# Kernel tuning notes

Hardware: AMD Instinct MI355X
Metric: run time of the kernel (lower is better)

Reference implementation:

```python
import jax, jax.numpy as jnp
import numpy as np

B, C, CO = 8, 32, 32            # batch, in_channels, out_channels
NIN, NOUT, D1, D2 = 16, 10, 512, 512  # MLP dims: 16 -> 512 -> 512 -> 10 (L=3)
NRC = (NIN + 2 * NOUT + 6) * C  # rc_inp feature dim = 42*C = 1344


def _conv1(x, W, b):
    # 1x1 Conv1d: x (b, Cin, N) -> (b, Cout, N)
    return jnp.einsum('oi,bin->bon', W, x) + b[None, :, None]


def _lin(x, W, b):
    return x @ W.T + b


def setup_inputs() -> dict:
    key = jax.random.key(0)
    ks = iter(jax.random.split(key, 64))
    def rn(shape, s=1.0):
        return jax.random.normal(next(ks), shape, dtype=jnp.float32) * s
    return {
        'w0': rn((B, C, D1, NIN)), 'w1': rn((B, C, D2, D1)), 'w2': rn((B, C, NOUT, D2)),
        'b0': rn((B, C, D1)), 'b1': rn((B, C, D2)), 'b2': rn((B, C, NOUT)),
        'W_w0_rpt': rn((NIN * CO, (NIN + 2) * C), 0.02), 'B_w0_rpt': rn((NIN * CO,), 0.02),
        'W_w0_rc': rn((NIN * CO, NRC), 0.02), 'B_w0_rc': rn((NIN * CO,), 0.02),
        'W_b0': rn((CO, (NIN + 2) * C), 0.02), 'B_b0': rn((CO,), 0.02),
        'W_b0_rc': rn((CO, NRC), 0.02), 'B_b0_rc': rn((CO,), 0.02),
        'W_l1': rn((CO, C), 0.02), 'B_l1': rn((CO,), 0.02),
        'W_l1_rc': rn((CO, NRC), 0.02), 'B_l1_rc': rn((CO,), 0.02),
        'W_l1_r': rn((CO, (3 + NIN) * C), 0.02), 'B_l1_r': rn((CO,), 0.02),
        'W_l1_c': rn((CO, (3 + NOUT) * C), 0.02), 'B_l1_c': rn((CO,), 0.02),
        'W_bias1': rn((CO, (3 + NOUT) * C), 0.02), 'B_bias1': rn((CO,), 0.02),
        'W_bias1_rc': rn((CO, NRC), 0.02), 'B_bias1_rc': rn((CO,), 0.02),
        'W_fin_cpt': rn((NOUT * CO, (NOUT + 1) * C), 0.02), 'B_fin_cpt': rn((NOUT * CO,), 0.02),
        'W_fin_rc': rn((NOUT * CO, NRC), 0.02), 'B_fin_rc': rn((NOUT * CO,), 0.02),
        'W_bfin_rc': rn((NOUT * CO, NRC), 0.02), 'B_bfin_rc': rn((NOUT * CO,), 0.02),
    }


def reference(w0, w1, w2, b0, b1, b2,
              W_w0_rpt, B_w0_rpt, W_w0_rc, B_w0_rc, W_b0, B_b0, W_b0_rc, B_b0_rc,
              W_l1, B_l1, W_l1_rc, B_l1_rc, W_l1_r, B_l1_r, W_l1_c, B_l1_c,
              W_bias1, B_bias1, W_bias1_rc, B_bias1_rc,
              W_fin_cpt, B_fin_cpt, W_fin_rc, B_fin_rc, W_bfin_rc, B_bfin_rc):
    b = w0.shape[0]
    cm0, cm1, cm2 = w0.mean(-1), w1.mean(-1), w2.mean(-1)  # col means (b,c,n_row)
    rm0, rm1, rm2 = w0.mean(-2), w1.mean(-2), w2.mean(-2)  # row means (b,c,n_col)
    rc = jnp.concatenate([
        w0.mean((-1, -2)), w1.mean((-1, -2)), w2.mean((-1, -2)),
        b0.mean(-1), b1.mean(-1), b2.mean(-1),
        rm0.reshape(b, -1), cm2.reshape(b, -1), b2.reshape(b, -1)], axis=-1)  # (b, NRC)
    # ---- layer 0 (row-pointwise + rc broadcast) ----
    rpt = jnp.concatenate([jnp.swapaxes(w0, -1, -2).reshape(b, C * NIN, D1), rm1, b0], axis=1)
    z0 = _conv1(rpt, W_w0_rpt, B_w0_rpt) + _lin(rc, W_w0_rc, B_w0_rc)[..., None]
    zw0 = jnp.swapaxes(z0.reshape(b, CO, NIN, D1), -1, -2)  # (b, co, D1, NIN)
    u0 = _conv1(rpt, W_b0, B_b0) + _lin(rc, W_b0_rc, B_b0_rc)[..., None]  # (b, co, D1)
    # ---- middle layer (pointwise + rc + row + col broadcasts) ----
    row_b = jnp.concatenate([rm1, cm0, b0, jnp.swapaxes(w0, -1, -2).reshape(b, C * NIN, D1)], axis=1)
    col_b = jnp.concatenate([cm1, b1, rm2, w2.reshape(b, C * NOUT, D2)], axis=1)
    zw1 = (jnp.einsum('oi,bihw->bohw', W_l1, w1) + B_l1[None, :, None, None]
           + _lin(rc, W_l1_rc, B_l1_rc)[..., None, None]
           + _conv1(row_b, W_l1_r, B_l1_r)[:, :, None, :]
           + _conv1(col_b, W_l1_c, B_l1_c)[:, :, :, None])  # (b, co, D2, D1)
    u1 = _conv1(col_b, W_bias1, B_bias1) + _lin(rc, W_bias1_rc, B_bias1_rc)[..., None]  # (b, co, D2)
    # ---- final layer (col-pointwise + rc broadcast) ----
    cpt = jnp.concatenate([w2.reshape(b, C * NOUT, D2), cm1], axis=1)
    zf = _conv1(cpt, W_fin_cpt, B_fin_cpt) + _lin(rc, W_fin_rc, B_fin_rc)[..., None]
    zw2 = zf.reshape(b, CO, NOUT, D2)
    u2 = _lin(rc, W_bfin_rc, B_bfin_rc).reshape(b, CO, NOUT)
    return (zw0, zw1, zw2, u0, u1, u2)
```

## Files before the change

### kernel.cpp

```cpp
#include <hip/hip_runtime.h>

#define OUT_ZW1 2097152u
#define OUT_ZW2 69206016u
#define OUT_U0  70516736u
#define OUT_U1  70647808u
#define OUT_U2  70778880u

#define WS_RM1P   0u
#define WS_CM1    524288u
#define WS_CM0    655360u
#define WS_RM2    786432u
#define WS_RCW1   917504u
#define WS_RC     918528u
#define WS_RTERM  929280u
#define WS_CTERM  1060352u
#define WS_W0T    1191424u
#define WS_TW0    3288576u
#define WS_TB0    3292672u
#define WS_TL1    3292928u
#define WS_TBIAS1 3293184u
#define WS_TFIN   3293440u

static __device__ __forceinline__ float wave_reduce(float v) {
#pragma unroll
  for (int off = 32; off > 0; off >>= 1) v += __shfl_down(v, off);
  return v;
}

__global__ __launch_bounds__(256) void ksetup(
    const float* __restrict__ w0, const float* __restrict__ w2,
    const float* __restrict__ b0, const float* __restrict__ b1,
    const float* __restrict__ b2, const float* __restrict__ w1,
    float* __restrict__ ws) {
  __shared__ float sred[16];
  __shared__ float stot;
  __shared__ float rpart[512];
  __shared__ float swsum[4];
  int tid = threadIdx.x, lane = tid & 63;
  int bx = blockIdx.x;

  if (bx < 256) {
    int bc = bx;
    int b = bc >> 5, c = bc & 31;
    float* rcb = ws + WS_RC + b * 1344;
    float* cm0 = ws + WS_CM0;
    float* rm2 = ws + WS_RM2;

    if (tid < 16) sred[tid] = 0.f;
    if (tid == 0) stot = 0.f;
    __syncthreads();
    {
      float rm0p[16];
#pragma unroll
      for (int k = 0; k < 16; ++k) rm0p[k] = 0.f;
      float tot = 0.f;
      for (int d = tid; d < 512; d += 256) {
        const float4* p = (const float4*)(w0 + ((size_t)bc * 512 + d) * 16);
        float s = 0.f;
#pragma unroll
        for (int q = 0; q < 4; ++q) {
          float4 v = p[q];
          s += v.x + v.y + v.z + v.w;
          rm0p[q * 4 + 0] += v.x; rm0p[q * 4 + 1] += v.y;
          rm0p[q * 4 + 2] += v.z; rm0p[q * 4 + 3] += v.w;
        }
        cm0[(size_t)bc * 512 + d] = s * (1.f / 16.f);
        tot += s;
      }
#pragma unroll
      for (int k = 0; k < 16; ++k) {
        float r = wave_reduce(rm0p[k]);
        if (lane == 0) atomicAdd(&sred[k], r);
      }
      float rt = wave_reduce(tot);
      if (lane == 0) atomicAdd(&stot, rt);
    }
    __syncthreads();
    if (tid < 16) rcb[192 + c * 16 + tid] = sred[tid] * (1.f / 512.f);
    if (tid == 0) rcb[c] = stot * (1.f / 8192.f);
    __syncthreads();

    if (tid < 10) sred[tid] = 0.f;
    if (tid == 0) stot = 0.f;
    __syncthreads();
    {
      float cm2p[10];
#pragma unroll
      for (int k = 0; k < 10; ++k) cm2p[k] = 0.f;
      float tot = 0.f;
      for (int d = tid; d < 512; d += 256) {
        float s = 0.f;
#pragma unroll
        for (int k = 0; k < 10; ++k) {
          float v = w2[((size_t)bc * 10 + k) * 512 + d];
          s += v; cm2p[k] += v;
        }
        rm2[(size_t)bc * 512 + d] = s * 0.1f;
        tot += s;
      }
#pragma unroll
      for (int k = 0; k < 10; ++k) {
        float r = wave_reduce(cm2p[k]);
        if (lane == 0) atomicAdd(&sred[k], r);
      }
      float rt = wave_reduce(tot);
      if (lane == 0) atomicAdd(&stot, rt);
    }
    __syncthreads();
    if (tid < 10) rcb[704 + c * 10 + tid] = sred[tid] * (1.f / 512.f);
    if (tid == 0) rcb[64 + c] = stot * (1.f / 5120.f);
    __syncthreads();

    if (tid < 2) sred[tid] = 0.f;
    __syncthreads();
    {
      float t0 = 0.f, t1 = 0.f;
      for (int d = tid; d < 512; d += 256) {
        t0 += b0[(size_t)bc * 512 + d];
        t1 += b1[(size_t)bc * 512 + d];
      }
      t0 = wave_reduce(t0); t1 = wave_reduce(t1);
      if (lane == 0) { atomicAdd(&sred[0], t0); atomicAdd(&sred[1], t1); }
    }
    __syncthreads();
    if (tid == 0) {
      rcb[96 + c] = sred[0] * (1.f / 512.f);
      rcb[128 + c] = sred[1] * (1.f / 512.f);
    }

    float vb2 = 0.f;
    if (tid < 10) {
      vb2 = b2[bc * 10 + tid];
      rcb[1024 + c * 10 + tid] = vb2;
    }
    if (tid < 64) {
      float s = wave_reduce(vb2);
      if (tid == 0) rcb[160 + c] = s * 0.1f;
    }
  } else if (bx < 1280) {
    int idx = bx - 256;
    int bc = idx >> 2, hc = idx & 3;
    int wid = tid >> 6;
    const float* base = w1 + (size_t)bc * 262144 + (size_t)hc * 65536;
    float col0 = 0.f, col1 = 0.f;
    for (int hl = 0; hl < 128; ++hl) {
      float2 x = *(const float2*)(base + hl * 512 + 2 * tid);
      col0 += x.x; col1 += x.y;
      float r = wave_reduce(x.x + x.y);
      if (lane == 0) rpart[hl * 4 + wid] = r;
    }
    __syncthreads();
    if (tid < 128) {
      float s = rpart[tid * 4] + rpart[tid * 4 + 1] + rpart[tid * 4 + 2] + rpart[tid * 4 + 3];
      ws[WS_CM1 + (size_t)bc * 512 + hc * 128 + tid] = s * (1.f / 512.f);
    }
    ws[WS_RM1P + (size_t)hc * 131072 + (size_t)bc * 512 + 2 * tid] = col0;
    ws[WS_RM1P + (size_t)hc * 131072 + (size_t)bc * 512 + 2 * tid + 1] = col1;
    float bt = wave_reduce(col0 + col1);
    if (lane == 0) swsum[wid] = bt;
    __syncthreads();
    if (tid == 0)
      ws[WS_RCW1 + hc * 256 + bc] = swsum[0] + swsum[1] + swsum[2] + swsum[3];
  } else {
    int bc = bx - 1280;
    int b = bc >> 5, c = bc & 31;
    for (int dd = 0; dd < 2; ++dd) {
      int d = tid + dd * 256;
      const float4* src = (const float4*)(w0 + ((size_t)bc * 512 + d) * 16);
      float4 v0 = src[0], v1 = src[1], v2 = src[2], v3 = src[3];
      float vals[16] = {v0.x, v0.y, v0.z, v0.w, v1.x, v1.y, v1.z, v1.w,
                        v2.x, v2.y, v2.z, v2.w, v3.x, v3.y, v3.z, v3.w};
#pragma unroll
      for (int k = 0; k < 16; ++k)
        ws[WS_W0T + ((size_t)(b * 512 + c * 16 + k)) * 512 + d] = vals[k];
    }
  }
}

__global__ __launch_bounds__(256) void krcgemm(
    float* __restrict__ ws,
    const float* __restrict__ W_w0_rc, const float* __restrict__ B_w0_rc,
    const float* __restrict__ W_b0_rc, const float* __restrict__ B_b0_rc,
    const float* __restrict__ W_l1_rc, const float* __restrict__ B_l1_rc,
    const float* __restrict__ W_bias1_rc, const float* __restrict__ B_bias1_rc,
    const float* __restrict__ W_fin_rc, const float* __restrict__ B_fin_rc,
    const float* __restrict__ W_bfin_rc, const float* __restrict__ B_bfin_rc,
    float* __restrict__ u2out) {
  int blk = blockIdx.x, tid = threadIdx.x;
  if (blk >= 2496) {
    int i = (blk - 2496) * 256 + tid;
    ws[WS_RM1P + i] = ws[WS_RM1P + i] + ws[WS_RM1P + 131072 + i] +
                      ws[WS_RM1P + 262144 + i] + ws[WS_RM1P + 393216 + i];
    return;
  }
  int b = blk / 312;
  int lane = tid & 63, wid = tid >> 6;
  int r = (blk % 312) * 4 + wid;
  __shared__ float rcs[1344];
  for (int j = tid; j < 1344; j += 256)
    if (j < 32 || j >= 64) rcs[j] = ws[WS_RC + b * 1344 + j];
  if (tid < 32)
    rcs[32 + tid] = (ws[WS_RCW1 + 0 * 256 + b * 32 + tid] +
                     ws[WS_RCW1 + 1 * 256 + b * 32 + tid] +
                     ws[WS_RCW1 + 2 * 256 + b * 32 + tid] +
                     ws[WS_RCW1 + 3 * 256 + b * 32 + tid]) * (1.f / 262144.f);
  __syncthreads();
  const float* W; const float* Bb; float* dst; int row;
  if (r < 512)      { W = W_w0_rc;    Bb = B_w0_rc;    row = r;       dst = ws + WS_TW0 + b * 512; }
  else if (r < 544) { W = W_b0_rc;    Bb = B_b0_rc;    row = r - 512; dst = ws + WS_TB0 + b * 32; }
  else if (r < 576) { W = W_l1_rc;    Bb = B_l1_rc;    row = r - 544; dst = ws + WS_TL1 + b * 32; }
  else if (r < 608) { W = W_bias1_rc; Bb = B_bias1_rc; row = r - 576; dst = ws + WS_TBIAS1 + b * 32; }
  else if (r < 928) { W = W_fin_rc;   Bb = B_fin_rc;   row = r - 608; dst = ws + WS_TFIN + b * 320; }
  else              { W = W_bfin_rc;  Bb = B_bfin_rc;  row = r - 928; dst = u2out + b * 320; }
  const float* wr = W + (size_t)row * 1344;
  float acc = 0.f;
  for (int j = lane; j < 1344; j += 64) acc += wr[j] * rcs[j];
  acc = wave_reduce(acc);
  if (lane == 0) dst[row] = acc + Bb[row];
}

__global__ __launch_bounds__(256) void kbig(
    const float* __restrict__ rm1, const float* __restrict__ cm0,
    const float* __restrict__ b0, const float* __restrict__ w0T,
    const float* __restrict__ W_l1_r, const float* __restrict__ B_l1_r,
    float* __restrict__ rterm,
    const float* __restrict__ cm1, const float* __restrict__ b1,
    const float* __restrict__ rm2, const float* __restrict__ w2,
    const float* __restrict__ W_l1_c, const float* __restrict__ B_l1_c,
    const float* __restrict__ B_l1, const float* __restrict__ t_l1,
    const float* __restrict__ W_bias1, const float* __restrict__ B_bias1,
    const float* __restrict__ t_bias1,
    float* __restrict__ cterm_full, float* __restrict__ u1out,
    const float* __restrict__ W_w0_rpt, const float* __restrict__ B_rpt,
    const float* __restrict__ W_b0, const float* __restrict__ B_b0w,
    const float* __restrict__ t_w0, const float* __restrict__ t_b0,
    const float* __restrict__ W_fin_cpt, const float* __restrict__ B_fin,
    const float* __restrict__ t_fin, float* __restrict__ out) {
  __shared__ float wlds[6656];
  int bid = blockIdx.x, tid = threadIdx.x;

  if (bid < 128) {
    int x = bid & 1, oy = (bid >> 1) & 7, b = bid >> 4;
    int p = x * 256 + tid;
    if (oy < 4) {
      int o0 = oy * 8;
      for (int idx = tid; idx < 608 * 8; idx += 256) {
        int i = idx >> 3, oo = idx & 7;
        wlds[idx] = W_l1_r[(size_t)(o0 + oo) * 608 + i];
      }
      __syncthreads();
      float acc[8] = {0, 0, 0, 0, 0, 0, 0, 0};
#pragma unroll 4
      for (int i = 0; i < 32; ++i) {
        float xv = rm1[((size_t)b * 32 + i) * 512 + p] * (1.f / 512.f);
        float4 wa = *(const float4*)&wlds[i * 8];
        float4 wb = *(const float4*)&wlds[i * 8 + 4];
        acc[0] += wa.x * xv; acc[1] += wa.y * xv; acc[2] += wa.z * xv; acc[3] += wa.w * xv;
        acc[4] += wb.x * xv; acc[5] += wb.y * xv; acc[6] += wb.z * xv; acc[7] += wb.w * xv;
      }
#pragma unroll 4
      for (int i = 0; i < 32; ++i) {
        float xv = cm0[((size_t)b * 32 + i) * 512 + p];
        float4 wa = *(const float4*)&wlds[(32 + i) * 8];
        float4 wb = *(const float4*)&wlds[(32 + i) * 8 + 4];
        acc[0] += wa.x * xv; acc[1] += wa.y * xv; acc[2] += wa.z * xv; acc[3] += wa.w * xv;
        acc[4] += wb.x * xv; acc[5] += wb.y * xv; acc[6] += wb.z * xv; acc[7] += wb.w * xv;
      }
#pragma unroll 4
      for (int i = 0; i < 32; ++i) {
        float xv = b0[((size_t)b * 32 + i) * 512 + p];
        float4 wa = *(const float4*)&wlds[(64 + i) * 8];
        float4 wb = *(const float4*)&wlds[(64 + i) * 8 + 4];
        acc[0] += wa.x * xv; acc[1] += wa.y * xv; acc[2] += wa.z * xv; acc[3] += wa.w * xv;
        acc[4] += wb.x * xv; acc[5] += wb.y * xv; acc[6] += wb.z * xv; acc[7] += wb.w * xv;
      }
      const float* xp = w0T + (size_t)b * 512 * 512 + p;
#pragma unroll 4
      for (int i = 0; i < 512; ++i) {
        float xv = xp[(size_t)i * 512];
        float4 wa = *(const float4*)&wlds[(96 + i) * 8];
        float4 wb = *(const float4*)&wlds[(96 + i) * 8 + 4];
        acc[0] += wa.x * xv; acc[1] += wa.y * xv; acc[2] += wa.z * xv; acc[3] += wa.w * xv;
        acc[4] += wb.x * xv; acc[5] += wb.y * xv; acc[6] += wb.z * xv; acc[7] += wb.w * xv;
      }
#pragma unroll
      for (int oo = 0; oo < 8; ++oo) {
        int o = o0 + oo;
        rterm[((size_t)b * 32 + o) * 512 + p] = acc[oo] + B_l1_r[o];
      }
    } else {
      int o0 = (oy - 4) * 8;
      for (int idx = tid; idx < 416 * 8; idx += 256) {
        int i = idx >> 3, oo = idx & 7;
        wlds[idx] = W_l1_c[(size_t)(o0 + oo) * 416 + i];
        wlds[3328 + idx] = W_bias1[(size_t)(o0 + oo) * 416 + i];
      }
      __syncthreads();
      float ac[8] = {0, 0, 0, 0, 0, 0, 0, 0};
      float au[8] = {0, 0, 0, 0, 0, 0, 0, 0};
#pragma unroll 4
      for (int i = 0; i < 32; ++i) {
        float xv = cm1[((size_t)b * 32 + i) * 512 + p];
        float4 wa = *(const float4*)&wlds[i * 8];
        float4 wb = *(const float4*)&wlds[i * 8 + 4];
        float4 va = *(const float4*)&wlds[3328 + i * 8];
        float4 vb = *(const float4*)&wlds[3328 + i * 8 + 4];
        ac[0] += wa.x * xv; ac[1] += wa.y * xv; ac[2] += wa.z * xv; ac[3] += wa.w * xv;
        ac[4] += wb.x * xv; ac[5] += wb.y * xv; ac[6] += wb.z * xv; ac[7] += wb.w * xv;
        au[0] += va.x * xv; au[1] += va.y * xv; au[2] += va.z * xv; au[3] += va.w * xv;
        au[4] += vb.x * xv; au[5] += vb.y * xv; au[6] += vb.z * xv; au[7] += vb.w * xv;
      }
#pragma unroll 4
      for (int i = 0; i < 32; ++i) {
        float xv = b1[((size_t)b * 32 + i) * 512 + p];
        float4 wa = *(const float4*)&wlds[(32 + i) * 8];
        float4 wb = *(const float4*)&wlds[(32 + i) * 8 + 4];
        float4 va = *(const float4*)&wlds[3328 + (32 + i) * 8];
        float4 vb = *(const float4*)&wlds[3328 + (32 + i) * 8 + 4];
        ac[0] += wa.x * xv; ac[1] += wa.y * xv; ac[2] += wa.z * xv; ac[3] += wa.w * xv;
        ac[4] += wb.x * xv; ac[5] += wb.y * xv; ac[6] += wb.z * xv; ac[7] += wb.w * xv;
        au[0] += va.x * xv; au[1] += va.y * xv; au[2] += va.z * xv; au[3] += va.w * xv;
        au[4] += vb.x * xv; au[5] += vb.y * xv; au[6] += vb.z * xv; au[7] += vb.w * xv;
      }
#pragma unroll 4
      for (int i = 0; i < 32; ++i) {
        float xv = rm2[((size_t)b * 32 + i) * 512 + p];
        float4 wa = *(const float4*)&wlds[(64 + i) * 8];
        float4 wb = *(const float4*)&wlds[(64 + i) * 8 + 4];
        float4 va = *(const float4*)&wlds[3328 + (64 + i) * 8];
        float4 vb = *(const float4*)&wlds[3328 + (64 + i) * 8 + 4];
        ac[0] += wa.x * xv; ac[1] += wa.y * xv; ac[2] += wa.z * xv; ac[3] += wa.w * xv;
        ac[4] += wb.x * xv; ac[5] += wb.y * xv; ac[6] += wb.z * xv; ac[7] += wb.w * xv;
        au[0] += va.x * xv; au[1] += va.y * xv; au[2] += va.z * xv; au[3] += va.w * xv;
        au[4] += vb.x * xv; au[5] += vb.y * xv; au[6] += vb.z * xv; au[7] += vb.w * xv;
      }
      const float* xp = w2 + (size_t)b * 320 * 512 + p;
#pragma unroll 4
      for (int i = 0; i < 320; ++i) {
        float xv = xp[(size_t)i * 512];
        float4 wa = *(const float4*)&wlds[(96 + i) * 8];
        float4 wb = *(const float4*)&wlds[(96 + i) * 8 + 4];
        float4 va = *(const float4*)&wlds[3328 + (96 + i) * 8];
        float4 vb = *(const float4*)&wlds[3328 + (96 + i) * 8 + 4];
        ac[0] += wa.x * xv; ac[1] += wa.y * xv; ac[2] += wa.z * xv; ac[3] += wa.w * xv;
        ac[4] += wb.x * xv; ac[5] += wb.y * xv; ac[6] += wb.z * xv; ac[7] += wb.w * xv;
        au[0] += va.x * xv; au[1] += va.y * xv; au[2] += va.z * xv; au[3] += va.w * xv;
        au[4] += vb.x * xv; au[5] += vb.y * xv; au[6] += vb.z * xv; au[7] += vb.w * xv;
      }
#pragma unroll
      for (int oo = 0; oo < 8; ++oo) {
        int o = o0 + oo;
        cterm_full[((size_t)b * 32 + o) * 512 + p] = ac[oo] + B_l1_c[o] + B_l1[o] + t_l1[b * 32 + o];
        u1out[((size_t)b * 32 + o) * 512 + p] = au[oo] + B_bias1[o] + t_bias1[b * 32 + o];
      }
    }
  } else if (bid < 1216) {
    int t = bid - 128;
    int x = t & 1, rest = t >> 1;
    int oc = rest % 68, b = rest / 68;
    bool isZ = oc < 64;
    int o0 = isZ ? oc * 8 : (oc - 64) * 8;
    const float* Wsrc = isZ ? W_w0_rpt : W_b0;
    for (int idx = tid; idx < 576 * 8; idx += 256) {
      int i = idx >> 3, oo = idx & 7;
      wlds[idx] = Wsrc[(size_t)(o0 + oo) * 576 + i];
    }
    __syncthreads();
    int d = x * 256 + tid;
    float acc[8] = {0, 0, 0, 0, 0, 0, 0, 0};
    const float* xp = w0T + (size_t)b * 512 * 512 + d;
#pragma unroll 4
    for (int i = 0; i < 512; ++i) {
      float xv = xp[(size_t)i * 512];
      float4 wa = *(const float4*)&wlds[i * 8];
      float4 wb = *(const float4*)&wlds[i * 8 + 4];
      acc[0] += wa.x * xv; acc[1] += wa.y * xv; acc[2] += wa.z * xv; acc[3] += wa.w * xv;
      acc[4] += wb.x * xv; acc[5] += wb.y * xv; acc[6] += wb.z * xv; acc[7] += wb.w * xv;
    }
#pragma unroll 4
    for (int i = 0; i < 32; ++i) {
      float xv = rm1[((size_t)b * 32 + i) * 512 + d] * (1.f / 512.f);
      float4 wa = *(const float4*)&wlds[(512 + i) * 8];
      float4 wb = *(const float4*)&wlds[(512 + i) * 8 + 4];
      acc[0] += wa.x * xv; acc[1] += wa.y * xv; acc[2] += wa.z * xv; acc[3] += wa.w * xv;
      acc[4] += wb.x * xv; acc[5] += wb.y * xv; acc[6] += wb.z * xv; acc[7] += wb.w * xv;
    }
#pragma unroll 4
    for (int i = 0; i < 32; ++i) {
      float xv = b0[((size_t)b * 32 + i) * 512 + d];
      float4 wa = *(const float4*)&wlds[(544 + i) * 8];
      float4 wb = *(const float4*)&wlds[(544 + i) * 8 + 4];
      acc[0] += wa.x * xv; acc[1] += wa.y * xv; acc[2] += wa.z * xv; acc[3] += wa.w * xv;
      acc[4] += wb.x * xv; acc[5] += wb.y * xv; acc[6] += wb.z * xv; acc[7] += wb.w * xv;
    }
    if (isZ) {
#pragma unroll
      for (int oo = 0; oo < 8; ++oo) {
        int o = o0 + oo, co = o >> 4, k = o & 15;
        out[(((size_t)b * 32 + co) * 512 + d) * 16 + k] = acc[oo] + B_rpt[o] + t_w0[b * 512 + o];
      }
    } else {
#pragma unroll
      for (int oo = 0; oo < 8; ++oo) {
        int o = o0 + oo;
        out[OUT_U0 + ((size_t)b * 32 + o) * 512 + d] = acc[oo] + B_b0w[o] + t_b0[b * 32 + o];
      }
    }
  } else {
    int t = bid - 1216;
    int x = t & 1, rest = t >> 1;
    int oc = rest % 40, b = rest / 40;
    int o0 = oc * 8;
    for (int idx = tid; idx < 352 * 8; idx += 256) {
      int i = idx >> 3, oo = idx & 7;
      wlds[idx] = W_fin_cpt[(size_t)(o0 + oo) * 352 + i];
    }
    __syncthreads();
    int d = x * 256 + tid;
    float acc[8] = {0, 0, 0, 0, 0, 0, 0, 0};
    const float* xp = w2 + (size_t)b * 320 * 512 + d;
#pragma unroll 4
    for (int i = 0; i < 320; ++i) {
      float xv = xp[(size_t)i * 512];
      float4 wa = *(const float4*)&wlds[i * 8];
      float4 wb = *(const float4*)&wlds[i * 8 + 4];
      acc[0] += wa.x * xv; acc[1] += wa.y * xv; acc[2] += wa.z * xv; acc[3] += wa.w * xv;
      acc[4] += wb.x * xv; acc[5] += wb.y * xv; acc[6] += wb.z * xv; acc[7] += wb.w * xv;
    }
#pragma unroll 4
    for (int i = 0; i < 32; ++i) {
      float xv = cm1[((size_t)b * 32 + i) * 512 + d];
      float4 wa = *(const float4*)&wlds[(320 + i) * 8];
      float4 wb = *(const float4*)&wlds[(320 + i) * 8 + 4];
      acc[0] += wa.x * xv; acc[1] += wa.y * xv; acc[2] += wa.z * xv; acc[3] += wa.w * xv;
      acc[4] += wb.x * xv; acc[5] += wb.y * xv; acc[6] += wb.z * xv; acc[7] += wb.w * xv;
    }
#pragma unroll
    for (int oo = 0; oo < 8; ++oo) {
      int o = o0 + oo;
      out[OUT_ZW2 + ((size_t)b * 320 + o) * 512 + d] = acc[oo] + B_fin[o] + t_fin[b * 320 + o];
    }
  }
}

__global__ __launch_bounds__(256) void kzw1(
    const float* __restrict__ w1, const float* __restrict__ W_l1,
    const float* __restrict__ rterm, const float* __restrict__ cterm,
    float* __restrict__ out) {
  __shared__ float wl[1024];
  int hp = blockIdx.x, b = blockIdx.y;
  int t = threadIdx.x;
  for (int i = t; i < 1024; i += 256) wl[(i & 31) * 32 + (i >> 5)] = W_l1[i];
  __syncthreads();
  int h0 = hp * 2;
  int hoff = t >> 7;
  int w = (t & 127) * 4;
  float4 acc[32];
#pragma unroll
  for (int o = 0; o < 32; ++o) acc[o] = make_float4(0.f, 0.f, 0.f, 0.f);
  const float* src = w1 + ((size_t)b * 32 * 512 + h0) * 512 + 4 * t;
#pragma unroll 4
  for (int i = 0; i < 32; ++i) {
    float4 x = *(const float4*)(src + (size_t)i * 262144);
    const float* wp = wl + i * 32;
#pragma unroll
    for (int o = 0; o < 32; ++o) {
      acc[o].x += wp[o] * x.x;
      acc[o].y += wp[o] * x.y;
      acc[o].z += wp[o] * x.z;
      acc[o].w += wp[o] * x.w;
    }
  }
  int h = h0 + hoff;
#pragma unroll
  for (int o = 0; o < 32; ++o) {
    float cf = cterm[((size_t)b * 32 + o) * 512 + h];
    float4 rt = *(const float4*)(rterm + ((size_t)b * 32 + o) * 512 + w);
    float4 res = make_float4(acc[o].x + rt.x + cf, acc[o].y + rt.y + cf,
                             acc[o].z + rt.z + cf, acc[o].w + rt.w + cf);
    *(float4*)(out + (size_t)OUT_ZW1 + (((size_t)b * 32 + o) * 512 + h) * 512 + w) = res;
  }
}

extern "C" void kernel_launch(void* const* d_in, const int* in_sizes, int n_in,
                              void* d_out, int out_size, void* d_ws, size_t ws_size,
                              hipStream_t stream) {
  const float* w0 = (const float*)d_in[0];
  const float* w1 = (const float*)d_in[1];
  const float* w2 = (const float*)d_in[2];
  const float* b0 = (const float*)d_in[3];
  const float* b1 = (const float*)d_in[4];
  const float* b2 = (const float*)d_in[5];
  const float* W_w0_rpt = (const float*)d_in[6];
  const float* B_w0_rpt = (const float*)d_in[7];
  const float* W_w0_rc = (const float*)d_in[8];
  const float* B_w0_rc = (const float*)d_in[9];
  const float* W_b0 = (const float*)d_in[10];
  const float* B_b0 = (const float*)d_in[11];
  const float* W_b0_rc = (const float*)d_in[12];
  const float* B_b0_rc = (const float*)d_in[13];
  const float* W_l1 = (const float*)d_in[14];
  const float* B_l1 = (const float*)d_in[15];
  const float* W_l1_rc = (const float*)d_in[16];
  const float* B_l1_rc = (const float*)d_in[17];
  const float* W_l1_r = (const float*)d_in[18];
  const float* B_l1_r = (const float*)d_in[19];
  const float* W_l1_c = (const float*)d_in[20];
  const float* B_l1_c = (const float*)d_in[21];
  const float* W_bias1 = (const float*)d_in[22];
  const float* B_bias1 = (const float*)d_in[23];
  const float* W_bias1_rc = (const float*)d_in[24];
  const float* B_bias1_rc = (const float*)d_in[25];
  const float* W_fin_cpt = (const float*)d_in[26];
  const float* B_fin_cpt = (const float*)d_in[27];
  const float* W_fin_rc = (const float*)d_in[28];
  const float* B_fin_rc = (const float*)d_in[29];
  const float* W_bfin_rc = (const float*)d_in[30];
  const float* B_bfin_rc = (const float*)d_in[31];
  float* ws = (float*)d_ws;
  float* out = (float*)d_out;

  ksetup<<<dim3(1536), 256, 0, stream>>>(w0, w2, b0, b1, b2, w1, ws);

  krcgemm<<<dim3(3008), 256, 0, stream>>>(
      ws, W_w0_rc, B_w0_rc, W_b0_rc, B_b0_rc, W_l1_rc, B_l1_rc, W_bias1_rc,
      B_bias1_rc, W_fin_rc, B_fin_rc, W_bfin_rc, B_bfin_rc, out + OUT_U2);

  kbig<<<dim3(1856), 256, 0, stream>>>(
      ws + WS_RM1P, ws + WS_CM0, b0, ws + WS_W0T, W_l1_r, B_l1_r, ws + WS_RTERM,
      ws + WS_CM1, b1, ws + WS_RM2, w2, W_l1_c, B_l1_c, B_l1, ws + WS_TL1, W_bias1,
      B_bias1, ws + WS_TBIAS1, ws + WS_CTERM, out + OUT_U1,
      W_w0_rpt, B_w0_rpt, W_b0, B_b0, ws + WS_TW0, ws + WS_TB0,
      W_fin_cpt, B_fin_cpt, ws + WS_TFIN, out);

  kzw1<<<dim3(256, 8), 256, 0, stream>>>(w1, W_l1, ws + WS_RTERM, ws + WS_CTERM, out);
  (void)in_sizes; (void)n_in; (void)out_size; (void)ws_size;
}
```

Measured before the change: 360.7 us.

## Replace scalar FP32 conv GEMMs with bf16 MFMA GEMM over packed panels

Setup now packs the activations and weights into bf16 panels, staged in the not-yet-written zw1 region of the output buffer. The four FP32 per-thread GEMM branches are replaced by one tiled kernel that computes 64x64 tiles with 16x16x32 bf16 MFMA instructions. The aim is to move the conv-style GEMMs from scalar FMAs onto matrix cores and to halve the operand bytes read. In exchange, precision drops to bf16 on inputs, and the LDS transpose store of the B tile may cause bank conflicts.

```diff
diff --git a/kernel.cpp b/kernel.cpp
--- a/kernel.cpp
+++ b/kernel.cpp
@@ -1,4 +1,8 @@
 #include <hip/hip_runtime.h>
+
+typedef unsigned short ushortT;
+typedef __attribute__((ext_vector_type(8))) short bf16x8;
+typedef __attribute__((ext_vector_type(4))) float f32x4;
 
 #define OUT_ZW1 2097152u
 #define OUT_ZW2 69206016u
@@ -7,31 +11,45 @@
 #define OUT_U2  70778880u
 
 #define WS_RM1P   0u
-#define WS_CM1    524288u
-#define WS_CM0    655360u
-#define WS_RM2    786432u
 #define WS_RCW1   917504u
 #define WS_RC     918528u
 #define WS_RTERM  929280u
 #define WS_CTERM  1060352u
-#define WS_W0T    1191424u
 #define WS_TW0    3288576u
 #define WS_TB0    3292672u
 #define WS_TL1    3292928u
 #define WS_TBIAS1 3293184u
 #define WS_TFIN   3293440u
 
+#define PZ0  0u
+#define PRT  2359296u
+#define PCT  4849664u
+#define PZF  6553600u
+#define PWZ0 7995392u
+#define PWRT 8308736u
+#define PWCT 8328192u
+#define PWZF 8354816u
+
 static __device__ __forceinline__ float wave_reduce(float v) {
 #pragma unroll
   for (int off = 32; off > 0; off >>= 1) v += __shfl_down(v, off);
   return v;
+}
+
+static __device__ __forceinline__ ushortT f2bf(float f) {
+  unsigned u = __float_as_uint(f);
+  u += 0x7FFFu + ((u >> 16) & 1u);
+  return (ushortT)(u >> 16);
 }
 
 __global__ __launch_bounds__(256) void ksetup(
     const float* __restrict__ w0, const float* __restrict__ w2,
     const float* __restrict__ b0, const float* __restrict__ b1,
     const float* __restrict__ b2, const float* __restrict__ w1,
-    float* __restrict__ ws) {
+    const float* __restrict__ W_w0_rpt, const float* __restrict__ W_b0,
+    const float* __restrict__ W_l1_r, const float* __restrict__ W_l1_c,
+    const float* __restrict__ W_bias1, const float* __restrict__ W_fin_cpt,
+    float* __restrict__ ws, ushortT* __restrict__ pan) {
   __shared__ float sred[16];
   __shared__ float stot;
   __shared__ float rpart[512];
@@ -43,8 +61,6 @@
     int bc = bx;
     int b = bc >> 5, c = bc & 31;
     float* rcb = ws + WS_RC + b * 1344;
-    float* cm0 = ws + WS_CM0;
-    float* rm2 = ws + WS_RM2;
 
     if (tid < 16) sred[tid] = 0.f;
     if (tid == 0) stot = 0.f;
@@ -64,7 +80,7 @@
           rm0p[q * 4 + 0] += v.x; rm0p[q * 4 + 1] += v.y;
           rm0p[q * 4 + 2] += v.z; rm0p[q * 4 + 3] += v.w;
         }
-        cm0[(size_t)bc * 512 + d] = s * (1.f / 16.f);
+        pan[PRT + ((size_t)(b * 608 + 32 + c)) * 512 + d] = f2bf(s * (1.f / 16.f));
         tot += s;
       }
 #pragma unroll
@@ -94,8 +110,11 @@
         for (int k = 0; k < 10; ++k) {
           float v = w2[((size_t)bc * 10 + k) * 512 + d];
           s += v; cm2p[k] += v;
+          ushortT bv = f2bf(v);
+          pan[PCT + ((size_t)(b * 416 + 96 + c * 10 + k)) * 512 + d] = bv;
+          pan[PZF + ((size_t)(b * 352 + c * 10 + k)) * 512 + d] = bv;
         }
-        rm2[(size_t)bc * 512 + d] = s * 0.1f;
+        pan[PCT + ((size_t)(b * 416 + 64 + c)) * 512 + d] = f2bf(s * 0.1f);
         tot += s;
       }
 #pragma unroll
@@ -116,8 +135,13 @@
     {
       float t0 = 0.f, t1 = 0.f;
       for (int d = tid; d < 512; d += 256) {
-        t0 += b0[(size_t)bc * 512 + d];
-        t1 += b1[(size_t)bc * 512 + d];
+        float vb0 = b0[(size_t)bc * 512 + d];
+        float vb1 = b1[(size_t)bc * 512 + d];
+        t0 += vb0; t1 += vb1;
+        ushortT h0 = f2bf(vb0);
+        pan[PRT + ((size_t)(b * 608 + 64 + c)) * 512 + d] = h0;
+        pan[PZ0 + ((size_t)(b * 576 + 544 + c)) * 512 + d] = h0;
+        pan[PCT + ((size_t)(b * 416 + 32 + c)) * 512 + d] = f2bf(vb1);
       }
       t0 = wave_reduce(t0); t1 = wave_reduce(t1);
       if (lane == 0) { atomicAdd(&sred[0], t0); atomicAdd(&sred[1], t1); }
@@ -140,6 +164,7 @@
   } else if (bx < 1280) {
     int idx = bx - 256;
     int bc = idx >> 2, hc = idx & 3;
+    int b = bc >> 5, c = bc & 31;
     int wid = tid >> 6;
     const float* base = w1 + (size_t)bc * 262144 + (size_t)hc * 65536;
     float col0 = 0.f, col1 = 0.f;
@@ -152,7 +177,9 @@
     __syncthreads();
     if (tid < 128) {
       float s = rpart[tid * 4] + rpart[tid * 4 + 1] + rpart[tid * 4 + 2] + rpart[tid * 4 + 3];
-      ws[WS_CM1 + (size_t)bc * 512 + hc * 128 + tid] = s * (1.f / 512.f);
+      ushortT m = f2bf(s * (1.f / 512.f));
+      pan[PCT + ((size_t)(b * 416 + c)) * 512 + hc * 128 + tid] = m;
+      pan[PZF + ((size_t)(b * 352 + 320 + c)) * 512 + hc * 128 + tid] = m;
     }
     ws[WS_RM1P + (size_t)hc * 131072 + (size_t)bc * 512 + 2 * tid] = col0;
     ws[WS_RM1P + (size_t)hc * 131072 + (size_t)bc * 512 + 2 * tid + 1] = col1;
@@ -161,7 +188,7 @@
     __syncthreads();
     if (tid == 0)
       ws[WS_RCW1 + hc * 256 + bc] = swsum[0] + swsum[1] + swsum[2] + swsum[3];
-  } else {
+  } else if (bx < 1536) {
     int bc = bx - 1280;
     int b = bc >> 5, c = bc & 31;
     for (int dd = 0; dd < 2; ++dd) {
@@ -171,14 +198,36 @@
       float vals[16] = {v0.x, v0.y, v0.z, v0.w, v1.x, v1.y, v1.z, v1.w,
                         v2.x, v2.y, v2.z, v2.w, v3.x, v3.y, v3.z, v3.w};
 #pragma unroll
-      for (int k = 0; k < 16; ++k)
-        ws[WS_W0T + ((size_t)(b * 512 + c * 16 + k)) * 512 + d] = vals[k];
+      for (int k = 0; k < 16; ++k) {
+        ushortT h = f2bf(vals[k]);
+        pan[PZ0 + ((size_t)(b * 576 + c * 16 + k)) * 512 + d] = h;
+        pan[PRT + ((size_t)(b * 608 + 96 + c * 16 + k)) * 512 + d] = h;
+      }
+    }
+  } else {
+    int g = bx - 1536;
+    int idx = g * 256 + tid;
+    if (g < 1224) {
+      int o = idx / 576, kk = idx - o * 576;
+      float v = (o < 512) ? W_w0_rpt[idx] : W_b0[(size_t)(o - 512) * 576 + kk];
+      pan[PWZ0 + idx] = f2bf(v);
+    } else if (g < 1300) {
+      int j = idx - 313344;
+      pan[PWRT + j] = f2bf(W_l1_r[j]);
+    } else if (g < 1404) {
+      int j = idx - 332800;
+      int o = j / 416, kk = j - o * 416;
+      float v = (o < 32) ? W_l1_c[j] : W_bias1[(size_t)(o - 32) * 416 + kk];
+      pan[PWCT + j] = f2bf(v);
+    } else {
+      int j = idx - 359424;
+      pan[PWZF + j] = f2bf(W_fin_cpt[j]);
     }
   }
 }
 
 __global__ __launch_bounds__(256) void krcgemm(
-    float* __restrict__ ws,
+    float* __restrict__ ws, ushortT* __restrict__ pan,
     const float* __restrict__ W_w0_rc, const float* __restrict__ B_w0_rc,
     const float* __restrict__ W_b0_rc, const float* __restrict__ B_b0_rc,
     const float* __restrict__ W_l1_rc, const float* __restrict__ B_l1_rc,
@@ -189,13 +238,19 @@
   int blk = blockIdx.x, tid = threadIdx.x;
   if (blk >= 2496) {
     int i = (blk - 2496) * 256 + tid;
-    ws[WS_RM1P + i] = ws[WS_RM1P + i] + ws[WS_RM1P + 131072 + i] +
-                      ws[WS_RM1P + 262144 + i] + ws[WS_RM1P + 393216 + i];
+    int bc = i >> 9, d = i & 511;
+    int b = bc >> 5, c = bc & 31;
+    float s = ws[WS_RM1P + i] + ws[WS_RM1P + 131072 + i] +
+              ws[WS_RM1P + 262144 + i] + ws[WS_RM1P + 393216 + i];
+    ushortT m = f2bf(s * (1.f / 512.f));
+    pan[PZ0 + ((size_t)(b * 576 + 512 + c)) * 512 + d] = m;
+    pan[PRT + ((size_t)(b * 608 + c)) * 512 + d] = m;
     return;
   }
-  int b = blk / 312;
+  int b = blk & 7;
+  int rg = blk >> 3;
   int lane = tid & 63, wid = tid >> 6;
-  int r = (blk % 312) * 4 + wid;
+  int r = rg * 4 + wid;
   __shared__ float rcs[1344];
   for (int j = tid; j < 1344; j += 256)
     if (j < 32 || j >= 64) rcs[j] = ws[WS_RC + b * 1344 + j];
@@ -219,226 +274,94 @@
   if (lane == 0) dst[row] = acc + Bb[row];
 }
 
-__global__ __launch_bounds__(256) void kbig(
-    const float* __restrict__ rm1, const float* __restrict__ cm0,
-    const float* __restrict__ b0, const float* __restrict__ w0T,
-    const float* __restrict__ W_l1_r, const float* __restrict__ B_l1_r,
-    float* __restrict__ rterm,
-    const float* __restrict__ cm1, const float* __restrict__ b1,
-    const float* __restrict__ rm2, const float* __restrict__ w2,
-    const float* __restrict__ W_l1_c, const float* __restrict__ B_l1_c,
-    const float* __restrict__ B_l1, const float* __restrict__ t_l1,
-    const float* __restrict__ W_bias1, const float* __restrict__ B_bias1,
-    const float* __restrict__ t_bias1,
-    float* __restrict__ cterm_full, float* __restrict__ u1out,
-    const float* __restrict__ W_w0_rpt, const float* __restrict__ B_rpt,
-    const float* __restrict__ W_b0, const float* __restrict__ B_b0w,
-    const float* __restrict__ t_w0, const float* __restrict__ t_b0,
-    const float* __restrict__ W_fin_cpt, const float* __restrict__ B_fin,
-    const float* __restrict__ t_fin, float* __restrict__ out) {
-  __shared__ float wlds[6656];
+__global__ __launch_bounds__(256) void kgemm(
+    const ushortT* __restrict__ pan,
+    const float* __restrict__ B_rpt, const float* __restrict__ t_w0,
+    const float* __restrict__ B_b0w, const float* __restrict__ t_b0,
+    const float* __restrict__ B_l1_r,
+    const float* __restrict__ B_l1_c, const float* __restrict__ B_l1,
+    const float* __restrict__ t_l1,
+    const float* __restrict__ B_bias1, const float* __restrict__ t_bias1,
+    const float* __restrict__ B_fin, const float* __restrict__ t_fin,
+    float* __restrict__ rterm, float* __restrict__ cterm,
+    float* __restrict__ u1out, float* __restrict__ out) {
+  __shared__ __align__(16) ushortT als[64 * 40];
+  __shared__ __align__(16) ushortT bls[64 * 40];
   int bid = blockIdx.x, tid = threadIdx.x;
-
-  if (bid < 128) {
-    int x = bid & 1, oy = (bid >> 1) & 7, b = bid >> 4;
-    int p = x * 256 + tid;
-    if (oy < 4) {
-      int o0 = oy * 8;
-      for (int idx = tid; idx < 608 * 8; idx += 256) {
-        int i = idx >> 3, oo = idx & 7;
-        wlds[idx] = W_l1_r[(size_t)(o0 + oo) * 608 + i];
-      }
-      __syncthreads();
-      float acc[8] = {0, 0, 0, 0, 0, 0, 0, 0};
-#pragma unroll 4
-      for (int i = 0; i < 32; ++i) {
-        float xv = rm1[((size_t)b * 32 + i) * 512 + p] * (1.f / 512.f);
-        float4 wa = *(const float4*)&wlds[i * 8];
-        float4 wb = *(const float4*)&wlds[i * 8 + 4];
-        acc[0] += wa.x * xv; acc[1] += wa.y * xv; acc[2] += wa.z * xv; acc[3] += wa.w * xv;
-        acc[4] += wb.x * xv; acc[5] += wb.y * xv; acc[6] += wb.z * xv; acc[7] += wb.w * xv;
-      }
-#pragma unroll 4
-      for (int i = 0; i < 32; ++i) {
-        float xv = cm0[((size_t)b * 32 + i) * 512 + p];
-        float4 wa = *(const float4*)&wlds[(32 + i) * 8];
-        float4 wb = *(const float4*)&wlds[(32 + i) * 8 + 4];
-        acc[0] += wa.x * xv; acc[1] += wa.y * xv; acc[2] += wa.z * xv; acc[3] += wa.w * xv;
-        acc[4] += wb.x * xv; acc[5] += wb.y * xv; acc[6] += wb.z * xv; acc[7] += wb.w * xv;
-      }
-#pragma unroll 4
-      for (int i = 0; i < 32; ++i) {
-        float xv = b0[((size_t)b * 32 + i) * 512 + p];
-        float4 wa = *(const float4*)&wlds[(64 + i) * 8];
-        float4 wb = *(const float4*)&wlds[(64 + i) * 8 + 4];
-        acc[0] += wa.x * xv; acc[1] += wa.y * xv; acc[2] += wa.z * xv; acc[3] += wa.w * xv;
-        acc[4] += wb.x * xv; acc[5] += wb.y * xv; acc[6] += wb.z * xv; acc[7] += wb.w * xv;
-      }
-      const float* xp = w0T + (size_t)b * 512 * 512 + p;
-#pragma unroll 4
-      for (int i = 0; i < 512; ++i) {
-        float xv = xp[(size_t)i * 512];
-        float4 wa = *(const float4*)&wlds[(96 + i) * 8];
-        float4 wb = *(const float4*)&wlds[(96 + i) * 8 + 4];
-        acc[0] += wa.x * xv; acc[1] += wa.y * xv; acc[2] += wa.z * xv; acc[3] += wa.w * xv;
-        acc[4] += wb.x * xv; acc[5] += wb.y * xv; acc[6] += wb.z * xv; acc[7] += wb.w * xv;
-      }
-#pragma unroll
-      for (int oo = 0; oo < 8; ++oo) {
-        int o = o0 + oo;
-        rterm[((size_t)b * 32 + o) * 512 + p] = acc[oo] + B_l1_r[o];
-      }
-    } else {
-      int o0 = (oy - 4) * 8;
-      for (int idx = tid; idx < 416 * 8; idx += 256) {
-        int i = idx >> 3, oo = idx & 7;
-        wlds[idx] = W_l1_c[(size_t)(o0 + oo) * 416 + i];
-        wlds[3328 + idx] = W_bias1[(size_t)(o0 + oo) * 416 + i];
-      }
-      __syncthreads();
-      float ac[8] = {0, 0, 0, 0, 0, 0, 0, 0};
-      float au[8] = {0, 0, 0, 0, 0, 0, 0, 0};
-#pragma unroll 4
-      for (int i = 0; i < 32; ++i) {
-        float xv = cm1[((size_t)b * 32 + i) * 512 + p];
-        float4 wa = *(const float4*)&wlds[i * 8];
-        float4 wb = *(const float4*)&wlds[i * 8 + 4];
-        float4 va = *(const float4*)&wlds[3328 + i * 8];
-        float4 vb = *(const float4*)&wlds[3328 + i * 8 + 4];
-        ac[0] += wa.x * xv; ac[1] += wa.y * xv; ac[2] += wa.z * xv; ac[3] += wa.w * xv;
-        ac[4] += wb.x * xv; ac[5] += wb.y * xv; ac[6] += wb.z * xv; ac[7] += wb.w * xv;
-        au[0] += va.x * xv; au[1] += va.y * xv; au[2] += va.z * xv; au[3] += va.w * xv;
-        au[4] += vb.x * xv; au[5] += vb.y * xv; au[6] += vb.z * xv; au[7] += vb.w * xv;
-      }
-#pragma unroll 4
-      for (int i = 0; i < 32; ++i) {
-        float xv = b1[((size_t)b * 32 + i) * 512 + p];
-        float4 wa = *(const float4*)&wlds[(32 + i) * 8];
-        float4 wb = *(const float4*)&wlds[(32 + i) * 8 + 4];
-        float4 va = *(const float4*)&wlds[3328 + (32 + i) * 8];
-        float4 vb = *(const float4*)&wlds[3328 + (32 + i) * 8 + 4];
-        ac[0] += wa.x * xv; ac[1] += wa.y * xv; ac[2] += wa.z * xv; ac[3] += wa.w * xv;
-        ac[4] += wb.x * xv; ac[5] += wb.y * xv; ac[6] += wb.z * xv; ac[7] += wb.w * xv;
-        au[0] += va.x * xv; au[1] += va.y * xv; au[2] += va.z * xv; au[3] += va.w * xv;
-        au[4] += vb.x * xv; au[5] += vb.y * xv; au[6] += vb.z * xv; au[7] += vb.w * xv;
-      }
-#pragma unroll 4
-      for (int i = 0; i < 32; ++i) {
-        float xv = rm2[((size_t)b * 32 + i) * 512 + p];
-        float4 wa = *(const float4*)&wlds[(64 + i) * 8];
-        float4 wb = *(const float4*)&wlds[(64 + i) * 8 + 4];
-        float4 va = *(const float4*)&wlds[3328 + (64 + i) * 8];
-        float4 vb = *(const float4*)&wlds[3328 + (64 + i) * 8 + 4];
-        ac[0] += wa.x * xv; ac[1] += wa.y * xv; ac[2] += wa.z * xv; ac[3] += wa.w * xv;
-        ac[4] += wb.x * xv; ac[5] += wb.y * xv; ac[6] += wb.z * xv; ac[7] += wb.w * xv;
-        au[0] += va.x * xv; au[1] += va.y * xv; au[2] += va.z * xv; au[3] += va.w * xv;
-        au[4] += vb.x * xv; au[5] += vb.y * xv; au[6] += vb.z * xv; au[7] += vb.w * xv;
-      }
-      const float* xp = w2 + (size_t)b * 320 * 512 + p;
-#pragma unroll 4
-      for (int i = 0; i < 320; ++i) {
-        float xv = xp[(size_t)i * 512];
-        float4 wa = *(const float4*)&wlds[(96 + i) * 8];
-        float4 wb = *(const float4*)&wlds[(96 + i) * 8 + 4];
-        float4 va = *(const float4*)&wlds[3328 + (96 + i) * 8];
-        float4 vb = *(const float4*)&wlds[3328 + (96 + i) * 8 + 4];
-        ac[0] += wa.x * xv; ac[1] += wa.y * xv; ac[2] += wa.z * xv; ac[3] += wa.w * xv;
-        ac[4] += wb.x * xv; ac[5] += wb.y * xv; ac[6] += wb.z * xv; ac[7] += wb.w * xv;
-        au[0] += va.x * xv; au[1] += va.y * xv; au[2] += va.z * xv; au[3] += va.w * xv;
-        au[4] += vb.x * xv; au[5] += vb.y * xv; au[6] += vb.z * xv; au[7] += vb.w * xv;
-      }
-#pragma unroll
-      for (int oo = 0; oo < 8; ++oo) {
-        int o = o0 + oo;
-        cterm_full[((size_t)b * 32 + o) * 512 + p] = ac[oo] + B_l1_c[o] + B_l1[o] + t_l1[b * 32 + o];
-        u1out[((size_t)b * 32 + o) * 512 + p] = au[oo] + B_bias1[o] + t_bias1[b * 32 + o];
-      }
-    }
-  } else if (bid < 1216) {
-    int t = bid - 128;
-    int x = t & 1, rest = t >> 1;
-    int oc = rest % 68, b = rest / 68;
-    bool isZ = oc < 64;
-    int o0 = isZ ? oc * 8 : (oc - 64) * 8;
-    const float* Wsrc = isZ ? W_w0_rpt : W_b0;
-    for (int idx = tid; idx < 576 * 8; idx += 256) {
-      int i = idx >> 3, oo = idx & 7;
-      wlds[idx] = Wsrc[(size_t)(o0 + oo) * 576 + i];
-    }
-    __syncthreads();
-    int d = x * 256 + tid;
-    float acc[8] = {0, 0, 0, 0, 0, 0, 0, 0};
-    const float* xp = w0T + (size_t)b * 512 * 512 + d;
-#pragma unroll 4
-    for (int i = 0; i < 512; ++i) {
-      float xv = xp[(size_t)i * 512];
-      float4 wa = *(const float4*)&wlds[i * 8];
-      float4 wb = *(const float4*)&wlds[i * 8 + 4];
-      acc[0] += wa.x * xv; acc[1] += wa.y * xv; acc[2] += wa.z * xv; acc[3] += wa.w * xv;
-      acc[4] += wb.x * xv; acc[5] += wb.y * xv; acc[6] += wb.z * xv; acc[7] += wb.w * xv;
-    }
-#pragma unroll 4
-    for (int i = 0; i < 32; ++i) {
-      float xv = rm1[((size_t)b * 32 + i) * 512 + d] * (1.f / 512.f);
-      float4 wa = *(const float4*)&wlds[(512 + i) * 8];
-      float4 wb = *(const float4*)&wlds[(512 + i) * 8 + 4];
-      acc[0] += wa.x * xv; acc[1] += wa.y * xv; acc[2] += wa.z * xv; acc[3] += wa.w * xv;
-      acc[4] += wb.x * xv; acc[5] += wb.y * xv; acc[6] += wb.z * xv; acc[7] += wb.w * xv;
-    }
-#pragma unroll 4
-    for (int i = 0; i < 32; ++i) {
-      float xv = b0[((size_t)b * 32 + i) * 512 + d];
-      float4 wa = *(const float4*)&wlds[(544 + i) * 8];
-      float4 wb = *(const float4*)&wlds[(544 + i) * 8 + 4];
-      acc[0] += wa.x * xv; acc[1] += wa.y * xv; acc[2] += wa.z * xv; acc[3] += wa.w * xv;
-      acc[4] += wb.x * xv; acc[5] += wb.y * xv; acc[6] += wb.z * xv; acc[7] += wb.w * xv;
-    }
-    if (isZ) {
-#pragma unroll
-      for (int oo = 0; oo < 8; ++oo) {
-        int o = o0 + oo, co = o >> 4, k = o & 15;
-        out[(((size_t)b * 32 + co) * 512 + d) * 16 + k] = acc[oo] + B_rpt[o] + t_w0[b * 512 + o];
-      }
-    } else {
-#pragma unroll
-      for (int oo = 0; oo < 8; ++oo) {
-        int o = o0 + oo;
-        out[OUT_U0 + ((size_t)b * 32 + o) * 512 + d] = acc[oo] + B_b0w[o] + t_b0[b * 32 + o];
-      }
-    }
+  int w = tid >> 6, lane = tid & 63;
+
+  const ushortT *X, *W;
+  int K, M, o0, d0, b, mode;
+  if (bid < 576) {
+    int t = bid; b = t & 7; int r = t >> 3; int mt = r % 9, dt = r / 9;
+    X = pan + PZ0 + (size_t)b * 576 * 512; W = pan + PWZ0;
+    K = 576; M = 544; o0 = mt * 64; d0 = dt * 64; mode = 0;
+  } else if (bid < 640) {
+    int t = bid - 576; b = t & 7; int dt = t >> 3;
+    X = pan + PRT + (size_t)b * 608 * 512; W = pan + PWRT;
+    K = 608; M = 32; o0 = 0; d0 = dt * 64; mode = 1;
+  } else if (bid < 704) {
+    int t = bid - 640; b = t & 7; int dt = t >> 3;
+    X = pan + PCT + (size_t)b * 416 * 512; W = pan + PWCT;
+    K = 416; M = 64; o0 = 0; d0 = dt * 64; mode = 2;
   } else {
-    int t = bid - 1216;
-    int x = t & 1, rest = t >> 1;
-    int oc = rest % 40, b = rest / 40;
-    int o0 = oc * 8;
-    for (int idx = tid; idx < 352 * 8; idx += 256) {
-      int i = idx >> 3, oo = idx & 7;
-      wlds[idx] = W_fin_cpt[(size_t)(o0 + oo) * 352 + i];
-    }
-    __syncthreads();
-    int d = x * 256 + tid;
-    float acc[8] = {0, 0, 0, 0, 0, 0, 0, 0};
-    const float* xp = w2 + (size_t)b * 320 * 512 + d;
-#pragma unroll 4
-    for (int i = 0; i < 320; ++i) {
-      float xv = xp[(size_t)i * 512];
-      float4 wa = *(const float4*)&wlds[i * 8];
-      float4 wb = *(const float4*)&wlds[i * 8 + 4];
-      acc[0] += wa.x * xv; acc[1] += wa.y * xv; acc[2] += wa.z * xv; acc[3] += wa.w * xv;
-      acc[4] += wb.x * xv; acc[5] += wb.y * xv; acc[6] += wb.z * xv; acc[7] += wb.w * xv;
-    }
-#pragma unroll 4
-    for (int i = 0; i < 32; ++i) {
-      float xv = cm1[((size_t)b * 32 + i) * 512 + d];
-      float4 wa = *(const float4*)&wlds[(320 + i) * 8];
-      float4 wb = *(const float4*)&wlds[(320 + i) * 8 + 4];
-      acc[0] += wa.x * xv; acc[1] += wa.y * xv; acc[2] += wa.z * xv; acc[3] += wa.w * xv;
-      acc[4] += wb.x * xv; acc[5] += wb.y * xv; acc[6] += wb.z * xv; acc[7] += wb.w * xv;
-    }
-#pragma unroll
-    for (int oo = 0; oo < 8; ++oo) {
-      int o = o0 + oo;
-      out[OUT_ZW2 + ((size_t)b * 320 + o) * 512 + d] = acc[oo] + B_fin[o] + t_fin[b * 320 + o];
+    int t = bid - 704; b = t & 7; int r = t >> 3; int mt = r % 5, dt = r / 5;
+    X = pan + PZF + (size_t)b * 352 * 512; W = pan + PWZF;
+    K = 352; M = 320; o0 = mt * 64; d0 = dt * 64; mode = 3;
+  }
+
+  f32x4 acc[4];
+#pragma unroll
+  for (int s = 0; s < 4; ++s) acc[s] = (f32x4){0.f, 0.f, 0.f, 0.f};
+
+  int ar = tid >> 2, ap = tid & 3;
+  int arow = o0 + ar; if (arow > M - 1) arow = M - 1;
+  int bk = tid >> 3, bg = tid & 7;
+
+  for (int kk = 0; kk < K; kk += 32) {
+    *(uint4*)&als[ar * 40 + ap * 8] = *(const uint4*)&W[(size_t)arow * K + kk + ap * 8];
+    uint4 v = *(const uint4*)&X[(size_t)(kk + bk) * 512 + d0 + bg * 8];
+    const ushortT* pv = (const ushortT*)&v;
+#pragma unroll
+    for (int jj = 0; jj < 8; ++jj) bls[(bg * 8 + jj) * 40 + bk] = pv[jj];
+    __syncthreads();
+    bf16x8 a = *(const bf16x8*)&als[(w * 16 + (lane & 15)) * 40 + (lane >> 4) * 8];
+#pragma unroll
+    for (int s = 0; s < 4; ++s) {
+      bf16x8 bb = *(const bf16x8*)&bls[(s * 16 + (lane & 15)) * 40 + (lane >> 4) * 8];
+      acc[s] = __builtin_amdgcn_mfma_f32_16x16x32_bf16(a, bb, acc[s], 0, 0, 0);
+    }
+    __syncthreads();
+  }
+
+  int col = lane & 15, rg2 = lane >> 4;
+#pragma unroll
+  for (int s = 0; s < 4; ++s) {
+    int d = d0 + s * 16 + col;
+#pragma unroll
+    for (int r = 0; r < 4; ++r) {
+      int o = o0 + w * 16 + rg2 * 4 + r;
+      float v = acc[s][r];
+      if (mode == 0) {
+        if (o < 512) {
+          int co = o >> 4, k2 = o & 15;
+          out[(((size_t)b * 32 + co) * 512 + d) * 16 + k2] = v + B_rpt[o] + t_w0[b * 512 + o];
+        } else if (o < 544) {
+          int oo = o - 512;
+          out[OUT_U0 + ((size_t)b * 32 + oo) * 512 + d] = v + B_b0w[oo] + t_b0[b * 32 + oo];
+        }
+      } else if (mode == 1) {
+        if (o < 32) rterm[((size_t)b * 32 + o) * 512 + d] = v + B_l1_r[o];
+      } else if (mode == 2) {
+        if (o < 32) {
+          cterm[((size_t)b * 32 + o) * 512 + d] = v + B_l1_c[o] + B_l1[o] + t_l1[b * 32 + o];
+        } else {
+          int oo = o - 32;
+          u1out[((size_t)b * 32 + oo) * 512 + d] = v + B_bias1[oo] + t_bias1[b * 32 + oo];
+        }
+      } else {
+        out[OUT_ZW2 + ((size_t)b * 320 + o) * 512 + d] = v + B_fin[o] + t_fin[b * 320 + o];
+      }
     }
   }
 }
@@ -519,19 +442,19 @@
   const float* B_bfin_rc = (const float*)d_in[31];
   float* ws = (float*)d_ws;
   float* out = (float*)d_out;
-
-  ksetup<<<dim3(1536), 256, 0, stream>>>(w0, w2, b0, b1, b2, w1, ws);
+  ushortT* pan = (ushortT*)(out + OUT_ZW1);
+
+  ksetup<<<dim3(3380), 256, 0, stream>>>(w0, w2, b0, b1, b2, w1, W_w0_rpt, W_b0,
+                                         W_l1_r, W_l1_c, W_bias1, W_fin_cpt, ws, pan);
 
   krcgemm<<<dim3(3008), 256, 0, stream>>>(
-      ws, W_w0_rc, B_w0_rc, W_b0_rc, B_b0_rc, W_l1_rc, B_l1_rc, W_bias1_rc,
+      ws, pan, W_w0_rc, B_w0_rc, W_b0_rc, B_b0_rc, W_l1_rc, B_l1_rc, W_bias1_rc,
       B_bias1_rc, W_fin_rc, B_fin_rc, W_bfin_rc, B_bfin_rc, out + OUT_U2);
 
-  kbig<<<dim3(1856), 256, 0, stream>>>(
-      ws + WS_RM1P, ws + WS_CM0, b0, ws + WS_W0T, W_l1_r, B_l1_r, ws + WS_RTERM,
-      ws + WS_CM1, b1, ws + WS_RM2, w2, W_l1_c, B_l1_c, B_l1, ws + WS_TL1, W_bias1,
-      B_bias1, ws + WS_TBIAS1, ws + WS_CTERM, out + OUT_U1,
-      W_w0_rpt, B_w0_rpt, W_b0, B_b0, ws + WS_TW0, ws + WS_TB0,
-      W_fin_cpt, B_fin_cpt, ws + WS_TFIN, out);
+  kgemm<<<dim3(1024), 256, 0, stream>>>(
+      pan, B_w0_rpt, ws + WS_TW0, B_b0, ws + WS_TB0, B_l1_r, B_l1_c, B_l1,
+      ws + WS_TL1, B_bias1, ws + WS_TBIAS1, B_fin_cpt, ws + WS_TFIN,
+      ws + WS_RTERM, ws + WS_CTERM, out + OUT_U1, out);
 
   kzw1<<<dim3(256, 8), 256, 0, stream>>>(w1, W_l1, ws + WS_RTERM, ws + WS_CTERM, out);
   (void)in_sizes; (void)n_in; (void)out_size; (void)ws_size;
```

Result: faster. 296.5 us (-17.8%).
